# Performance work log

Hardware: AMD Instinct MI355X
Metric: run time of the kernel (lower is better)

The kernel has to match this reference:

```python
import jax, jax.numpy as jnp
import numpy as np

VOCAB, EMBED = 100000, 128
B, QLEN, DLEN = 1024, 32, 256
KERNEL_NUM, SIGMA, EXACT_SIGMA = 11, 0.1, 0.001
EPS = 1e-8  # torch F.cosine_similarity eps


def _kernel_mus(n):
    l_mu = [1.0]
    if n == 1:
        return l_mu
    bin_size = 2.0 / (n - 1)
    l_mu.append(1 - bin_size / 2)
    for i in range(1, n - 1):
        l_mu.append(round(l_mu[i] - bin_size, 5))
    return list(reversed(l_mu))


def _kernel_sigmas(n, sigma, exact_sigma):
    l_sigma = [exact_sigma]
    if n == 1:
        return l_sigma
    l_sigma += [sigma] * (n - 1)
    return list(reversed(l_sigma))


MUS = jnp.asarray(np.array(_kernel_mus(KERNEL_NUM), dtype=np.float32))      # [K]
SIGMAS = jnp.asarray(np.array(_kernel_sigmas(KERNEL_NUM, SIGMA, EXACT_SIGMA), dtype=np.float32))  # [K]


def setup_inputs() -> dict:
    key = jax.random.key(0)
    k = jax.random.split(key, 7)
    return {
        "emb": jax.random.normal(k[0], (VOCAB, EMBED), dtype=jnp.float32),
        "mlp_w": jax.random.normal(k[1], (1, KERNEL_NUM), dtype=jnp.float32) * 0.3,
        "mlp_b": jax.random.normal(k[2], (1,), dtype=jnp.float32) * 0.1,
        "query1": jax.random.randint(k[3], (B, QLEN), 0, VOCAB, dtype=jnp.int32).astype(jnp.int64),
        "doc1": jax.random.randint(k[4], (B, DLEN), 0, VOCAB, dtype=jnp.int32).astype(jnp.int64),
        "query2": jax.random.randint(k[5], (B, QLEN), 0, VOCAB, dtype=jnp.int32).astype(jnp.int64),
        "doc2": jax.random.randint(k[6], (B, DLEN), 0, VOCAB, dtype=jnp.int32).astype(jnp.int64),
    }


def _predict(emb, mlp_w, mlp_b, query, doc):
    qe = emb[query]                               # [B,Q,E]
    de = emb[doc]                                 # [B,D,E]
    qn = jnp.linalg.norm(qe, axis=-1)             # [B,Q]
    dn = jnp.linalg.norm(de, axis=-1)             # [B,D]
    dots = jnp.einsum("bqe,bde->bqd", qe, de)    # [B,Q,D]
    sim = dots / jnp.maximum(qn[:, :, None] * dn[:, None, :], EPS)
    # multi-Gaussian soft histogram: exp(-(sim-mu)^2/(2 sigma^2)), sum over doc,
    # log1p, sum over query  -> [B,K]
    z = (sim[..., None] - MUS) / SIGMAS           # [B,Q,D,K]
    K = jnp.exp(-0.5 * z * z)
    pooled = jnp.log1p(K.sum(axis=2)).sum(axis=1)  # [B,K]
    return pooled @ mlp_w.T + mlp_b               # [B,1]


def reference(emb, mlp_w, mlp_b, query1, doc1, query2, doc2):
    logits_1 = _predict(emb, mlp_w, mlp_b, query1, doc1)
    logits_2 = _predict(emb, mlp_w, mlp_b, query2, doc2)
    return jax.nn.sigmoid(logits_1 - logits_2)    # [B,1]
```

## Files before the change

kernel.cpp:

```cpp
#include <hip/hip_runtime.h>
#include <math.h>

#define VOCAB 100000
#define NB    1024
#define QLEN  32
#define DLEN  256
#define EMBED 128
#define KNUM  11

typedef __attribute__((ext_vector_type(8))) short bf16x8;
typedef __attribute__((ext_vector_type(4))) float f32x4;

#define HALF_L2E 0.7213475204444817f
#define TWO_L2E  2.8853900817779268f
#define EM4      0.018315638888734179f

#define SSTR  68
#define SHALF (16 * SSTR)

__global__ __launch_bounds__(256)
void cvt_table(const float* __restrict__ emb, ushort* __restrict__ ebf,
               float* __restrict__ inorm)
{
    const int row = blockIdx.x * 8 + (threadIdx.x >> 5);
    const int l32 = threadIdx.x & 31;
    const float4 v = *((const float4*)(emb + (size_t)row * EMBED) + l32);
    union { float f; unsigned u; } x0, x1, x2, x3;
    x0.f = v.x; x1.f = v.y; x2.f = v.z; x3.f = v.w;
    const unsigned r0 = x0.u + 0x8000u, r1 = x1.u + 0x8000u;
    const unsigned r2 = x2.u + 0x8000u, r3 = x3.u + 0x8000u;
    uint2 packed;
    packed.x = (r0 >> 16) | (r1 & 0xFFFF0000u);
    packed.y = (r2 >> 16) | (r3 & 0xFFFF0000u);
    *((uint2*)(ebf + (size_t)row * EMBED) + l32) = packed;
    x0.u = r0 & 0xFFFF0000u; x1.u = r1 & 0xFFFF0000u;
    x2.u = r2 & 0xFFFF0000u; x3.u = r3 & 0xFFFF0000u;
    float n = x0.f * x0.f + x1.f * x1.f + x2.f * x2.f + x3.f * x3.f;
    #pragma unroll
    for (int m = 1; m < 32; m <<= 1) n += __shfl_xor(n, m);
    if (l32 == 0) inorm[row] = __builtin_amdgcn_rsqf(n);
}

__device__ __forceinline__ bf16x8 cvt8(const float* p, float& nacc)
{
    uint4 a = *((const uint4*)p);
    uint4 b = *((const uint4*)(p + 4));
    unsigned u[8] = {a.x, a.y, a.z, a.w, b.x, b.y, b.z, b.w};
    bf16x8 r;
    #pragma unroll
    for (int i = 0; i < 8; ++i) {
        const unsigned q = u[i] + 0x8000u;
        r[i] = (short)(q >> 16);
        union { unsigned uu; float ff; } g; g.uu = q & 0xFFFF0000u;
        nacc = fmaf(g.ff, g.ff, nacc);
    }
    return r;
}

template<bool PRE>
__global__ __launch_bounds__(256, 6)
void knrm_logits(const float* __restrict__ emb,
                 const ushort* __restrict__ ebf,
                 const float* __restrict__ inorm,
                 const float* __restrict__ mlp_w,
                 const int* __restrict__ q1, const int* __restrict__ d1,
                 const int* __restrict__ q2, const int* __restrict__ d2,
                 float* __restrict__ logits)
{
    const int b    = blockIdx.x;
    const int pair = blockIdx.y;
    const int t    = threadIdx.x;
    const int w    = t >> 6;
    const int lane = t & 63;
    const int l15  = lane & 15;
    const int quad = lane >> 4;

    const int* __restrict__ qry = (pair == 0 ? q1 : q2) + b * QLEN;
    const int* __restrict__ doc = (pair == 0 ? d1 : d2) + b * DLEN;

    __shared__ __align__(16) float s_sim[4 * SHALF];
    __shared__ float s_tot[QLEN][12];

    #pragma unroll
    for (int i = t; i < QLEN * 12; i += 256) ((float*)s_tot)[i] = 0.f;
    __syncthreads();

    const int qid0 = qry[l15];
    const int qid1 = qry[l15 + 16];
    int did[4];
    #pragma unroll
    for (int nt = 0; nt < 4; ++nt) did[nt] = doc[(w * 4 + nt) * 16 + l15];

    f32x4 acc[2][4];
    #pragma unroll
    for (int mt = 0; mt < 2; ++mt)
        #pragma unroll
        for (int nt = 0; nt < 4; ++nt)
            acc[mt][nt] = (f32x4){0.f, 0.f, 0.f, 0.f};

    float idn[4];
    float riqn[2][4];

    if (PRE) {
        const ushort* qp0 = ebf + (size_t)qid0 * EMBED + quad * 8;
        const ushort* qp1 = ebf + (size_t)qid1 * EMBED + quad * 8;
        #pragma unroll
        for (int kk = 0; kk < 4; ++kk) {
            const bf16x8 a0 = *((const bf16x8*)(qp0 + kk * 32));
            const bf16x8 a1 = *((const bf16x8*)(qp1 + kk * 32));
            #pragma unroll
            for (int nt = 0; nt < 4; ++nt) {
                const bf16x8 bb = *((const bf16x8*)(ebf + (size_t)did[nt] * EMBED + quad * 8 + kk * 32));
                acc[0][nt] = __builtin_amdgcn_mfma_f32_16x16x32_bf16(a0, bb, acc[0][nt], 0, 0, 0);
                acc[1][nt] = __builtin_amdgcn_mfma_f32_16x16x32_bf16(a1, bb, acc[1][nt], 0, 0, 0);
            }
        }
        #pragma unroll
        for (int nt = 0; nt < 4; ++nt) idn[nt] = inorm[did[nt]];
        #pragma unroll
        for (int r = 0; r < 4; ++r) {
            riqn[0][r] = inorm[qry[quad * 4 + r]];
            riqn[1][r] = inorm[qry[16 + quad * 4 + r]];
        }
    } else {
        float qn2[2] = {0.f, 0.f};
        float dn2[4] = {0.f, 0.f, 0.f, 0.f};
        const float* qp0 = emb + (size_t)qid0 * EMBED + quad * 8;
        const float* qp1 = emb + (size_t)qid1 * EMBED + quad * 8;
        #pragma unroll
        for (int kk = 0; kk < 4; ++kk) {
            const bf16x8 a0 = cvt8(qp0 + kk * 32, qn2[0]);
            const bf16x8 a1 = cvt8(qp1 + kk * 32, qn2[1]);
            #pragma unroll
            for (int nt = 0; nt < 4; ++nt) {
                const bf16x8 bb = cvt8(emb + (size_t)did[nt] * EMBED + quad * 8 + kk * 32, dn2[nt]);
                acc[0][nt] = __builtin_amdgcn_mfma_f32_16x16x32_bf16(a0, bb, acc[0][nt], 0, 0, 0);
                acc[1][nt] = __builtin_amdgcn_mfma_f32_16x16x32_bf16(a1, bb, acc[1][nt], 0, 0, 0);
            }
        }
        #pragma unroll
        for (int i = 0; i < 2; ++i) {
            qn2[i] += __shfl_xor(qn2[i], 16);
            qn2[i] += __shfl_xor(qn2[i], 32);
        }
        #pragma unroll
        for (int nt = 0; nt < 4; ++nt) {
            dn2[nt] += __shfl_xor(dn2[nt], 16);
            dn2[nt] += __shfl_xor(dn2[nt], 32);
            idn[nt] = __builtin_amdgcn_rsqf(dn2[nt]);
        }
        #pragma unroll
        for (int r = 0; r < 4; ++r) {
            riqn[0][r] = __builtin_amdgcn_rsqf(__shfl(qn2[0], quad * 4 + r));
            riqn[1][r] = __builtin_amdgcn_rsqf(__shfl(qn2[1], quad * 4 + r));
        }
    }

    float* wtile = s_sim + w * SHALF;
    const int m = l15;
    const int c = quad;

    #pragma unroll
    for (int mt = 0; mt < 2; ++mt) {
        #pragma unroll
        for (int nt = 0; nt < 4; ++nt)
            #pragma unroll
            for (int r = 0; r < 4; ++r)
                wtile[(quad * 4 + r) * SSTR + nt * 16 + l15] =
                    acc[mt][nt][r] * riqn[mt][r] * idn[nt];

        const float* rp = wtile + m * SSTR + c * 16;
        float ksum[KNUM];
        #pragma unroll
        for (int k = 0; k < KNUM; ++k) ksum[k] = 0.f;

        #pragma unroll
        for (int i = 0; i < 4; ++i) {
            const f32x4 sv = *((const f32x4*)(rp + 4 * i));
            #pragma unroll
            for (int e = 0; e < 4; ++e) {
                const float s  = sv[e];
                const float z  = fmaf(s, 10.f, -1.f);
                const float e0 = exp2f(-HALF_L2E * (z * z));
                float ru = exp2f(fmaf(z,  TWO_L2E, -TWO_L2E));
                float rd = exp2f(fmaf(z, -TWO_L2E, -TWO_L2E));
                ksum[5] += e0;
                float tt = e0;
                tt *= ru; ksum[6] += tt; ru *= EM4;
                tt *= ru; ksum[7] += tt; ru *= EM4;
                tt *= ru; ksum[8] += tt; ru *= EM4;
                tt *= ru; ksum[9] += tt;
                tt = e0;
                tt *= rd; ksum[4] += tt; rd *= EM4;
                tt *= rd; ksum[3] += tt; rd *= EM4;
                tt *= rd; ksum[2] += tt; rd *= EM4;
                tt *= rd; ksum[1] += tt; rd *= EM4;
                tt *= rd; ksum[0] += tt;
                ksum[10] += (s > 0.995f) ? 1.f : 0.f;
            }
        }

        #pragma unroll
        for (int k = 0; k < KNUM; ++k) {
            ksum[k] += __shfl_xor(ksum[k], 16);
            ksum[k] += __shfl_xor(ksum[k], 32);
        }
        if (quad == 0) {
            #pragma unroll
            for (int k = 0; k < KNUM; ++k)
                atomicAdd(&s_tot[mt * 16 + m][k], ksum[k]);
        }
    }
    __syncthreads();

    if (t < QLEN) {
        float contrib = 0.f;
        #pragma unroll
        for (int k = 0; k < KNUM; ++k)
            contrib += mlp_w[k] * log1pf(s_tot[t][k]);
        #pragma unroll
        for (int mm = 1; mm < 32; mm <<= 1) contrib += __shfl_xor(contrib, mm);
        if (t == 0) logits[pair * NB + b] = contrib;
    }
}

__global__ __launch_bounds__(256)
void knrm_combine(const float* __restrict__ logits, float* __restrict__ out)
{
    const int i = blockIdx.x * blockDim.x + threadIdx.x;
    if (i < NB) {
        const float d = logits[i] - logits[NB + i];
        out[i] = 1.f / (1.f + __expf(-d));
    }
}

extern "C" void kernel_launch(void* const* d_in, const int* in_sizes, int n_in,
                              void* d_out, int out_size, void* d_ws, size_t ws_size,
                              hipStream_t stream)
{
    const float* emb   = (const float*)d_in[0];
    const float* mlp_w = (const float*)d_in[1];
    const int* q1 = (const int*)d_in[3];
    const int* d1 = (const int*)d_in[4];
    const int* q2 = (const int*)d_in[5];
    const int* d2 = (const int*)d_in[6];

    float* out    = (float*)d_out;
    float* logits = (float*)d_ws;

    const size_t need = 2 * NB * 4
                      + (size_t)VOCAB * 4
                      + (size_t)VOCAB * EMBED * 2 + 256;
    dim3 grid(NB, 2);
    if (ws_size >= need) {
        float*  inorm = logits + 2 * NB;
        ushort* ebf   = (ushort*)(inorm + VOCAB);
        cvt_table<<<VOCAB / 8, 256, 0, stream>>>(emb, ebf, inorm);
        knrm_logits<true><<<grid, 256, 0, stream>>>(emb, ebf, inorm, mlp_w,
                                                    q1, d1, q2, d2, logits);
    } else {
        knrm_logits<false><<<grid, 256, 0, stream>>>(emb, nullptr, nullptr, mlp_w,
                                                     q1, d1, q2, d2, logits);
    }
    knrm_combine<<<(NB + 255) / 256, 256, 0, stream>>>(logits, out);
}
```

Measured before the change: 152.7 us.

## Fuse both query-doc pairs into one block and prefetch second pair during pooling

Result: faster. 145.8 us (-4.5%).

```diff
diff --git a/kernel.cpp b/kernel.cpp
--- a/kernel.cpp
+++ b/kernel.cpp
@@ -57,39 +57,97 @@
     return r;
 }
 
+__device__ __forceinline__ void pool_half(float* __restrict__ wtile,
+                                          const f32x4* __restrict__ a,
+                                          const float* __restrict__ riq,
+                                          const float* __restrict__ idn,
+                                          float (*__restrict__ stot)[12],
+                                          int mtbase, int l15, int quad)
+{
+    #pragma unroll
+    for (int nt = 0; nt < 4; ++nt)
+        #pragma unroll
+        for (int r = 0; r < 4; ++r)
+            wtile[(quad * 4 + r) * SSTR + nt * 16 + l15] = a[nt][r] * riq[r] * idn[nt];
+
+    const float* rp = wtile + l15 * SSTR + quad * 16;
+    float ksum[KNUM];
+    #pragma unroll
+    for (int k = 0; k < KNUM; ++k) ksum[k] = 0.f;
+
+    #pragma unroll
+    for (int i = 0; i < 4; ++i) {
+        const f32x4 sv = *((const f32x4*)(rp + 4 * i));
+        #pragma unroll
+        for (int e = 0; e < 4; ++e) {
+            const float s  = sv[e];
+            const float z  = fmaf(s, 10.f, -1.f);
+            const float e0 = exp2f(-HALF_L2E * (z * z));
+            float ru = exp2f(fmaf(z,  TWO_L2E, -TWO_L2E));
+            float rd = exp2f(fmaf(z, -TWO_L2E, -TWO_L2E));
+            ksum[5] += e0;
+            float tt = e0;
+            tt *= ru; ksum[6] += tt; ru *= EM4;
+            tt *= ru; ksum[7] += tt; ru *= EM4;
+            tt *= ru; ksum[8] += tt; ru *= EM4;
+            tt *= ru; ksum[9] += tt;
+            tt = e0;
+            tt *= rd; ksum[4] += tt; rd *= EM4;
+            tt *= rd; ksum[3] += tt; rd *= EM4;
+            tt *= rd; ksum[2] += tt; rd *= EM4;
+            tt *= rd; ksum[1] += tt; rd *= EM4;
+            tt *= rd; ksum[0] += tt;
+            ksum[10] += (s > 0.995f) ? 1.f : 0.f;
+        }
+    }
+    #pragma unroll
+    for (int k = 0; k < KNUM; ++k) {
+        ksum[k] += __shfl_xor(ksum[k], 16);
+        ksum[k] += __shfl_xor(ksum[k], 32);
+    }
+    if (quad == 0) {
+        #pragma unroll
+        for (int k = 0; k < KNUM; ++k)
+            atomicAdd(&stot[mtbase + l15][k], ksum[k]);
+    }
+}
+
 template<bool PRE>
-__global__ __launch_bounds__(256, 6)
-void knrm_logits(const float* __restrict__ emb,
-                 const ushort* __restrict__ ebf,
-                 const float* __restrict__ inorm,
-                 const float* __restrict__ mlp_w,
-                 const int* __restrict__ q1, const int* __restrict__ d1,
-                 const int* __restrict__ q2, const int* __restrict__ d2,
-                 float* __restrict__ logits)
+__global__ __launch_bounds__(256, 2)
+void knrm_fused(const float* __restrict__ emb,
+                const ushort* __restrict__ ebf,
+                const float* __restrict__ inorm,
+                const float* __restrict__ mlp_w,
+                const int* __restrict__ q1, const int* __restrict__ d1,
+                const int* __restrict__ q2, const int* __restrict__ d2,
+                float* __restrict__ out)
 {
     const int b    = blockIdx.x;
-    const int pair = blockIdx.y;
     const int t    = threadIdx.x;
     const int w    = t >> 6;
-    const int lane = t & 63;
-    const int l15  = lane & 15;
-    const int quad = lane >> 4;
-
-    const int* __restrict__ qry = (pair == 0 ? q1 : q2) + b * QLEN;
-    const int* __restrict__ doc = (pair == 0 ? d1 : d2) + b * DLEN;
+    const int l15  = t & 15;
+    const int quad = (t & 63) >> 4;
+
+    const int* __restrict__ qryA = q1 + b * QLEN;
+    const int* __restrict__ docA = d1 + b * DLEN;
+    const int* __restrict__ qryB = q2 + b * QLEN;
+    const int* __restrict__ docB = d2 + b * DLEN;
 
     __shared__ __align__(16) float s_sim[4 * SHALF];
-    __shared__ float s_tot[QLEN][12];
-
-    #pragma unroll
-    for (int i = t; i < QLEN * 12; i += 256) ((float*)s_tot)[i] = 0.f;
+    __shared__ float s_tot[2][QLEN][12];
+
+    #pragma unroll
+    for (int i = t; i < 2 * QLEN * 12; i += 256) ((float*)s_tot)[i] = 0.f;
     __syncthreads();
 
-    const int qid0 = qry[l15];
-    const int qid1 = qry[l15 + 16];
-    int did[4];
-    #pragma unroll
-    for (int nt = 0; nt < 4; ++nt) did[nt] = doc[(w * 4 + nt) * 16 + l15];
+    const int qidA0 = qryA[l15], qidA1 = qryA[l15 + 16];
+    const int qidB0 = qryB[l15], qidB1 = qryB[l15 + 16];
+    int didA[4], didB[4];
+    #pragma unroll
+    for (int nt = 0; nt < 4; ++nt) {
+        didA[nt] = docA[(w * 4 + nt) * 16 + l15];
+        didB[nt] = docB[(w * 4 + nt) * 16 + l15];
+    }
 
     f32x4 acc[2][4];
     #pragma unroll
@@ -98,139 +156,120 @@
         for (int nt = 0; nt < 4; ++nt)
             acc[mt][nt] = (f32x4){0.f, 0.f, 0.f, 0.f};
 
-    float idn[4];
-    float riqn[2][4];
+    float idnA[4], idnB[4], riqA[2][4], riqB[2][4];
+    float* wtile = s_sim + w * SHALF;
 
     if (PRE) {
-        const ushort* qp0 = ebf + (size_t)qid0 * EMBED + quad * 8;
-        const ushort* qp1 = ebf + (size_t)qid1 * EMBED + quad * 8;
+        const ushort* qa0 = ebf + (size_t)qidA0 * EMBED + quad * 8;
+        const ushort* qa1 = ebf + (size_t)qidA1 * EMBED + quad * 8;
         #pragma unroll
         for (int kk = 0; kk < 4; ++kk) {
-            const bf16x8 a0 = *((const bf16x8*)(qp0 + kk * 32));
-            const bf16x8 a1 = *((const bf16x8*)(qp1 + kk * 32));
+            const bf16x8 a0 = *((const bf16x8*)(qa0 + kk * 32));
+            const bf16x8 a1 = *((const bf16x8*)(qa1 + kk * 32));
             #pragma unroll
             for (int nt = 0; nt < 4; ++nt) {
-                const bf16x8 bb = *((const bf16x8*)(ebf + (size_t)did[nt] * EMBED + quad * 8 + kk * 32));
+                const bf16x8 bb = *((const bf16x8*)(ebf + (size_t)didA[nt] * EMBED + quad * 8 + kk * 32));
                 acc[0][nt] = __builtin_amdgcn_mfma_f32_16x16x32_bf16(a0, bb, acc[0][nt], 0, 0, 0);
                 acc[1][nt] = __builtin_amdgcn_mfma_f32_16x16x32_bf16(a1, bb, acc[1][nt], 0, 0, 0);
             }
         }
-        #pragma unroll
-        for (int nt = 0; nt < 4; ++nt) idn[nt] = inorm[did[nt]];
+
+        bf16x8 pq0[4], pq1[4], pdb[4][4];
+        const ushort* qb0 = ebf + (size_t)qidB0 * EMBED + quad * 8;
+        const ushort* qb1 = ebf + (size_t)qidB1 * EMBED + quad * 8;
+        #pragma unroll
+        for (int kk = 0; kk < 4; ++kk) {
+            pq0[kk] = *((const bf16x8*)(qb0 + kk * 32));
+            pq1[kk] = *((const bf16x8*)(qb1 + kk * 32));
+            #pragma unroll
+            for (int nt = 0; nt < 4; ++nt)
+                pdb[nt][kk] = *((const bf16x8*)(ebf + (size_t)didB[nt] * EMBED + quad * 8 + kk * 32));
+        }
+        #pragma unroll
+        for (int nt = 0; nt < 4; ++nt) { idnA[nt] = inorm[didA[nt]]; idnB[nt] = inorm[didB[nt]]; }
         #pragma unroll
         for (int r = 0; r < 4; ++r) {
-            riqn[0][r] = inorm[qry[quad * 4 + r]];
-            riqn[1][r] = inorm[qry[16 + quad * 4 + r]];
-        }
+            riqA[0][r] = inorm[qryA[quad * 4 + r]];
+            riqA[1][r] = inorm[qryA[16 + quad * 4 + r]];
+            riqB[0][r] = inorm[qryB[quad * 4 + r]];
+            riqB[1][r] = inorm[qryB[16 + quad * 4 + r]];
+        }
+
+        pool_half(wtile, acc[0], riqA[0], idnA, s_tot[0], 0,  l15, quad);
+        pool_half(wtile, acc[1], riqA[1], idnA, s_tot[0], 16, l15, quad);
+
+        #pragma unroll
+        for (int mt = 0; mt < 2; ++mt)
+            #pragma unroll
+            for (int nt = 0; nt < 4; ++nt)
+                acc[mt][nt] = (f32x4){0.f, 0.f, 0.f, 0.f};
+        #pragma unroll
+        for (int kk = 0; kk < 4; ++kk)
+            #pragma unroll
+            for (int nt = 0; nt < 4; ++nt) {
+                acc[0][nt] = __builtin_amdgcn_mfma_f32_16x16x32_bf16(pq0[kk], pdb[nt][kk], acc[0][nt], 0, 0, 0);
+                acc[1][nt] = __builtin_amdgcn_mfma_f32_16x16x32_bf16(pq1[kk], pdb[nt][kk], acc[1][nt], 0, 0, 0);
+            }
+
+        pool_half(wtile, acc[0], riqB[0], idnB, s_tot[1], 0,  l15, quad);
+        pool_half(wtile, acc[1], riqB[1], idnB, s_tot[1], 16, l15, quad);
     } else {
-        float qn2[2] = {0.f, 0.f};
-        float dn2[4] = {0.f, 0.f, 0.f, 0.f};
-        const float* qp0 = emb + (size_t)qid0 * EMBED + quad * 8;
-        const float* qp1 = emb + (size_t)qid1 * EMBED + quad * 8;
-        #pragma unroll
-        for (int kk = 0; kk < 4; ++kk) {
-            const bf16x8 a0 = cvt8(qp0 + kk * 32, qn2[0]);
-            const bf16x8 a1 = cvt8(qp1 + kk * 32, qn2[1]);
+        #pragma unroll
+        for (int p = 0; p < 2; ++p) {
+            const int* qry = p == 0 ? qryA : qryB;
+            const int qi0 = p == 0 ? qidA0 : qidB0;
+            const int qi1 = p == 0 ? qidA1 : qidB1;
+            const int* did = p == 0 ? didA : didB;
+            float qn2[2] = {0.f, 0.f}, dn2[4] = {0.f, 0.f, 0.f, 0.f};
+            #pragma unroll
+            for (int mt = 0; mt < 2; ++mt)
+                #pragma unroll
+                for (int nt = 0; nt < 4; ++nt)
+                    acc[mt][nt] = (f32x4){0.f, 0.f, 0.f, 0.f};
+            const float* qp0 = emb + (size_t)qi0 * EMBED + quad * 8;
+            const float* qp1 = emb + (size_t)qi1 * EMBED + quad * 8;
+            #pragma unroll
+            for (int kk = 0; kk < 4; ++kk) {
+                const bf16x8 a0 = cvt8(qp0 + kk * 32, qn2[0]);
+                const bf16x8 a1 = cvt8(qp1 + kk * 32, qn2[1]);
+                #pragma unroll
+                for (int nt = 0; nt < 4; ++nt) {
+                    const bf16x8 bb = cvt8(emb + (size_t)did[nt] * EMBED + quad * 8 + kk * 32, dn2[nt]);
+                    acc[0][nt] = __builtin_amdgcn_mfma_f32_16x16x32_bf16(a0, bb, acc[0][nt], 0, 0, 0);
+                    acc[1][nt] = __builtin_amdgcn_mfma_f32_16x16x32_bf16(a1, bb, acc[1][nt], 0, 0, 0);
+                }
+            }
+            float idn[4], riq[2][4];
+            #pragma unroll
+            for (int i = 0; i < 2; ++i) {
+                qn2[i] += __shfl_xor(qn2[i], 16);
+                qn2[i] += __shfl_xor(qn2[i], 32);
+            }
             #pragma unroll
             for (int nt = 0; nt < 4; ++nt) {
-                const bf16x8 bb = cvt8(emb + (size_t)did[nt] * EMBED + quad * 8 + kk * 32, dn2[nt]);
-                acc[0][nt] = __builtin_amdgcn_mfma_f32_16x16x32_bf16(a0, bb, acc[0][nt], 0, 0, 0);
-                acc[1][nt] = __builtin_amdgcn_mfma_f32_16x16x32_bf16(a1, bb, acc[1][nt], 0, 0, 0);
-            }
-        }
-        #pragma unroll
-        for (int i = 0; i < 2; ++i) {
-            qn2[i] += __shfl_xor(qn2[i], 16);
-            qn2[i] += __shfl_xor(qn2[i], 32);
-        }
-        #pragma unroll
-        for (int nt = 0; nt < 4; ++nt) {
-            dn2[nt] += __shfl_xor(dn2[nt], 16);
-            dn2[nt] += __shfl_xor(dn2[nt], 32);
-            idn[nt] = __builtin_amdgcn_rsqf(dn2[nt]);
-        }
-        #pragma unroll
-        for (int r = 0; r < 4; ++r) {
-            riqn[0][r] = __builtin_amdgcn_rsqf(__shfl(qn2[0], quad * 4 + r));
-            riqn[1][r] = __builtin_amdgcn_rsqf(__shfl(qn2[1], quad * 4 + r));
-        }
-    }
-
-    float* wtile = s_sim + w * SHALF;
-    const int m = l15;
-    const int c = quad;
-
-    #pragma unroll
-    for (int mt = 0; mt < 2; ++mt) {
-        #pragma unroll
-        for (int nt = 0; nt < 4; ++nt)
-            #pragma unroll
-            for (int r = 0; r < 4; ++r)
-                wtile[(quad * 4 + r) * SSTR + nt * 16 + l15] =
-                    acc[mt][nt][r] * riqn[mt][r] * idn[nt];
-
-        const float* rp = wtile + m * SSTR + c * 16;
-        float ksum[KNUM];
-        #pragma unroll
-        for (int k = 0; k < KNUM; ++k) ksum[k] = 0.f;
-
-        #pragma unroll
-        for (int i = 0; i < 4; ++i) {
-            const f32x4 sv = *((const f32x4*)(rp + 4 * i));
-            #pragma unroll
-            for (int e = 0; e < 4; ++e) {
-                const float s  = sv[e];
-                const float z  = fmaf(s, 10.f, -1.f);
-                const float e0 = exp2f(-HALF_L2E * (z * z));
-                float ru = exp2f(fmaf(z,  TWO_L2E, -TWO_L2E));
-                float rd = exp2f(fmaf(z, -TWO_L2E, -TWO_L2E));
-                ksum[5] += e0;
-                float tt = e0;
-                tt *= ru; ksum[6] += tt; ru *= EM4;
-                tt *= ru; ksum[7] += tt; ru *= EM4;
-                tt *= ru; ksum[8] += tt; ru *= EM4;
-                tt *= ru; ksum[9] += tt;
-                tt = e0;
-                tt *= rd; ksum[4] += tt; rd *= EM4;
-                tt *= rd; ksum[3] += tt; rd *= EM4;
-                tt *= rd; ksum[2] += tt; rd *= EM4;
-                tt *= rd; ksum[1] += tt; rd *= EM4;
-                tt *= rd; ksum[0] += tt;
-                ksum[10] += (s > 0.995f) ? 1.f : 0.f;
-            }
-        }
-
-        #pragma unroll
-        for (int k = 0; k < KNUM; ++k) {
-            ksum[k] += __shfl_xor(ksum[k], 16);
-            ksum[k] += __shfl_xor(ksum[k], 32);
-        }
-        if (quad == 0) {
-            #pragma unroll
-            for (int k = 0; k < KNUM; ++k)
-                atomicAdd(&s_tot[mt * 16 + m][k], ksum[k]);
+                dn2[nt] += __shfl_xor(dn2[nt], 16);
+                dn2[nt] += __shfl_xor(dn2[nt], 32);
+                idn[nt] = __builtin_amdgcn_rsqf(dn2[nt]);
+            }
+            #pragma unroll
+            for (int r = 0; r < 4; ++r) {
+                riq[0][r] = __builtin_amdgcn_rsqf(__shfl(qn2[0], quad * 4 + r));
+                riq[1][r] = __builtin_amdgcn_rsqf(__shfl(qn2[1], quad * 4 + r));
+            }
+            pool_half(wtile, acc[0], riq[0], idn, s_tot[p], 0,  l15, quad);
+            pool_half(wtile, acc[1], riq[1], idn, s_tot[p], 16, l15, quad);
         }
     }
     __syncthreads();
 
     if (t < QLEN) {
-        float contrib = 0.f;
+        float c = 0.f;
         #pragma unroll
         for (int k = 0; k < KNUM; ++k)
-            contrib += mlp_w[k] * log1pf(s_tot[t][k]);
-        #pragma unroll
-        for (int mm = 1; mm < 32; mm <<= 1) contrib += __shfl_xor(contrib, mm);
-        if (t == 0) logits[pair * NB + b] = contrib;
-    }
-}
-
-__global__ __launch_bounds__(256)
-void knrm_combine(const float* __restrict__ logits, float* __restrict__ out)
-{
-    const int i = blockIdx.x * blockDim.x + threadIdx.x;
-    if (i < NB) {
-        const float d = logits[i] - logits[NB + i];
-        out[i] = 1.f / (1.f + __expf(-d));
+            c += mlp_w[k] * (log1pf(s_tot[0][t][k]) - log1pf(s_tot[1][t][k]));
+        #pragma unroll
+        for (int mm = 1; mm < 32; mm <<= 1) c += __shfl_xor(c, mm);
+        if (t == 0) out[b] = 1.f / (1.f + __expf(-c));
     }
 }
 
@@ -245,22 +284,18 @@
     const int* q2 = (const int*)d_in[5];
     const int* d2 = (const int*)d_in[6];
 
-    float* out    = (float*)d_out;
-    float* logits = (float*)d_ws;
-
-    const size_t need = 2 * NB * 4
-                      + (size_t)VOCAB * 4
+    float* out = (float*)d_out;
+
+    const size_t need = (size_t)VOCAB * 4
                       + (size_t)VOCAB * EMBED * 2 + 256;
-    dim3 grid(NB, 2);
     if (ws_size >= need) {
-        float*  inorm = logits + 2 * NB;
+        float*  inorm = (float*)d_ws;
         ushort* ebf   = (ushort*)(inorm + VOCAB);
         cvt_table<<<VOCAB / 8, 256, 0, stream>>>(emb, ebf, inorm);
-        knrm_logits<true><<<grid, 256, 0, stream>>>(emb, ebf, inorm, mlp_w,
-                                                    q1, d1, q2, d2, logits);
+        knrm_fused<true><<<NB, 256, 0, stream>>>(emb, ebf, inorm, mlp_w,
+                                                 q1, d1, q2, d2, out);
     } else {
-        knrm_logits<false><<<grid, 256, 0, stream>>>(emb, nullptr, nullptr, mlp_w,
-                                                     q1, d1, q2, d2, logits);
-    }
-    knrm_combine<<<(NB + 255) / 256, 256, 0, stream>>>(logits, out);
-}
+        knrm_fused<false><<<NB, 256, 0, stream>>>(emb, nullptr, nullptr, mlp_w,
+                                                  q1, d1, q2, d2, out);
+    }
+}
```
